# Optimization experiments

Hardware: AMD Instinct MI355X
Metric: run time of the kernel (lower is better)

The kernel has to match this reference:

```python
import jax, jax.numpy as jnp
from jax import lax
import numpy as np

B, A, D = 4, 512, 729   # batch, num_angles, detector pixels
H, W = 512, 512         # reconstruction volume


def setup_inputs() -> dict:
    key = jax.random.key(0)
    sino = jax.random.normal(key, (B, A, D), dtype=jnp.float32)
    vol_spacing = np.array([1.0, 1.0], dtype=np.float32)          # (sy, sx)
    det_spacing = np.array([1.0], dtype=np.float32)
    vol_origin = np.array([-(H - 1) / 2.0, -(W - 1) / 2.0], dtype=np.float32)
    det_origin = np.array([-(D - 1) / 2.0], dtype=np.float32)
    angles = jnp.linspace(0.0, jnp.pi, A, endpoint=False, dtype=jnp.float32)
    return {
        "input": sino,
        "volume_shape": np.array([H, W], dtype=np.int64),
        "volume_origin": jnp.asarray(vol_origin),
        "detector_origin": jnp.asarray(det_origin),
        "volume_spacing": jnpp if False else jnp.asarray(vol_spacing),
        "detector_spacing": jnp.asarray(det_spacing),
        "trajectory": angles,
    }


def _backproject(sino, vol_shape, vol_origin, det_origin, vol_spacing, det_spacing, angles):
    h, w = int(vol_shape[0]), int(vol_shape[1])
    d = sino.shape[-1]
    ys = vol_origin[0] + jnp.arange(h, dtype=sino.dtype) * vol_spacing[0]  # [H]
    xs = vol_origin[1] + jnp.arange(w, dtype=sino.dtype) * vol_spacing[1]  # [W]

    def step(acc, per_angle):
        theta, sino_a = per_angle                      # scalar, [B, D]
        # ray coordinate s = x*cos(theta) + y*sin(theta) for every voxel
        s = xs[None, :] * jnp.cos(theta) + ys[:, None] * jnp.sin(theta)  # [H, W]
        u = (s - det_origin[0]) / det_spacing[0]       # continuous detector index
        u0 = jnp.floor(u)
        frac = u - u0
        i0 = u0.astype(jnp.int32)
        i1 = i0 + 1
        valid0 = (i0 >= 0) & (i0 < d)
        valid1 = (i1 >= 0) & (i1 < d)
        i0c = jnp.clip(i0, 0, d - 1)
        i1c = jnp.clip(i1, 0, d - 1)
        v0 = sino_a[:, i0c]                            # [B, H, W] gather
        v1 = sino_a[:, i1c]                            # [B, H, W] gather
        contrib = (jnp.where(valid0, (1.0 - frac) * v0, 0.0)
                   + jnp.where(valid1, frac * v1, 0.0))
        return acc + contrib, None

    acc0 = jnp.zeros((sino.shape[0], h, w), dtype=sino.dtype)
    out, _ = lax.scan(step, acc0, (angles, jnp.swapaxes(sino, 0, 1)))
    return out


def reference(input, volume_shape, volume_origin, detector_origin,
              volume_spacing, detector_spacing, trajectory):
    return _backproject(input, volume_shape, volume_origin, detector_origin,
                        volume_spacing, detector_spacing, trajectory)
```

## Files before the change

kernel.cpp:

```cpp
#include <hip/hip_runtime.h>

#define BB 4
#define AA 512
#define ZS 4
#define AH (AA / ZS)
#define DD 729
#define HH 512
#define WW 512
#define CH 8
#define WIN 32

typedef float f4v __attribute__((ext_vector_type(4)));

__device__ inline void gload_lds(const float* g, float* l) {
    __builtin_amdgcn_global_load_lds(
        (const __attribute__((address_space(1))) unsigned int*)g,
        (__attribute__((address_space(3))) unsigned int*)l, 4, 0, 0);
}

__global__ __launch_bounds__(128, 8) void bp_kernel(
    const float* __restrict__ sino,
    const float* __restrict__ vol_origin,
    const float* __restrict__ det_origin,
    const float* __restrict__ vol_spacing,
    const float* __restrict__ det_spacing,
    const float* __restrict__ angles,
    float* __restrict__ out)
{
    __shared__ f4v   s_csk[AH];
    __shared__ int   s_s0[AH];
    __shared__ float s_win[2][CH * WIN * BB];

    const int tid  = threadIdx.y * 16 + threadIdx.x;
    const int lane = tid & 63;
    const int wv   = tid >> 6;

    const float inv_ds = 1.0f / det_spacing[0];
    const int abase = blockIdx.z * AH;

    const int x0 = blockIdx.x * 16;
    const int y0 = blockIdx.y * 16;
    const float vsx = vol_spacing[1], vsy = vol_spacing[0];
    const float off = -det_origin[0] * inv_ds;
    const float xc = vol_origin[1] + ((float)x0 + 7.5f) * vsx;
    const float yc = vol_origin[0] + ((float)y0 + 7.5f) * vsy;

    for (int a = tid; a < AH; a += 128) {
        float th = angles[abase + a];
        float c = cosf(th) * inv_ds;
        float s = sinf(th) * inv_ds;
        float uc = fmaf(xc, c, fmaf(yc, s, off));
        int s0 = min(max((int)uc - (WIN / 2), 0), DD - WIN);
        f4v k;
        k.x = c; k.y = s; k.z = off - (float)s0; k.w = 8.0f * vsy * s;
        s_csk[a] = k;
        s_s0[a]  = s0;
    }
    __syncthreads();

    const int ix  = x0 + threadIdx.x;
    const int iyA = y0 + threadIdx.y;
    const float xw = vol_origin[1] + (float)ix * vsx;
    const float yw = vol_origin[0] + (float)iyA * vsy;

    const int sidx = wv * 64 + lane;
    const long sgoff = (long)(lane & 3) * (AA * DD) + (sidx >> 2);

    f4v accA = {0.f, 0.f, 0.f, 0.f};
    f4v accB = {0.f, 0.f, 0.f, 0.f};

    #define STAGE(A0, P)                                                   \
        do {                                                               \
            _Pragma("unroll")                                              \
            for (int i = 0; i < CH; ++i) {                                 \
                const int  s0  = s_s0[(A0) + i];                           \
                const long row = (long)(abase + (A0) + i) * DD + s0;       \
                gload_lds(sino + row + sgoff,                              \
                          &s_win[P][i * (WIN * BB) + wv * 64]);            \
            }                                                              \
        } while (0)

    int p = 0;
    STAGE(0, 0);
    for (int a0 = 0; a0 < AH; a0 += CH) {
        __syncthreads();
        if (a0 + CH < AH) STAGE(a0 + CH, p ^ 1);
        #pragma unroll
        for (int j = 0; j < CH; ++j) {
            const f4v  k  = s_csk[a0 + j];
            const float u0 = fmaf(xw, k.x, fmaf(yw, k.y, k.z));
            const float u1 = u0 + k.w;
            {
                const int   li = (int)u0;
                const float fr = __builtin_amdgcn_fractf(u0);
                const float om = 1.0f - fr;
                const f4v* w = (const f4v*)&s_win[p][(j * WIN + li) * BB];
                const f4v P = w[0], Q = w[1];
                const f4v fr4 = {fr, fr, fr, fr};
                const f4v om4 = {om, om, om, om};
                accA = accA + fr4 * Q + om4 * P;
            }
            {
                const int   li = (int)u1;
                const float fr = __builtin_amdgcn_fractf(u1);
                const float om = 1.0f - fr;
                const f4v* w = (const f4v*)&s_win[p][(j * WIN + li) * BB];
                const f4v P = w[0], Q = w[1];
                const f4v fr4 = {fr, fr, fr, fr};
                const f4v om4 = {om, om, om, om};
                accB = accB + fr4 * Q + om4 * P;
            }
        }
        p ^= 1;
    }
    #undef STAGE

    const size_t HW = (size_t)HH * WW;
    const size_t oA = (size_t)iyA * WW + ix;
    const size_t oB = oA + (size_t)8 * WW;
    unsafeAtomicAdd(&out[oA],          accA.x);
    unsafeAtomicAdd(&out[oA + HW],     accA.y);
    unsafeAtomicAdd(&out[oA + 2 * HW], accA.z);
    unsafeAtomicAdd(&out[oA + 3 * HW], accA.w);
    unsafeAtomicAdd(&out[oB],          accB.x);
    unsafeAtomicAdd(&out[oB + HW],     accB.y);
    unsafeAtomicAdd(&out[oB + 2 * HW], accB.z);
    unsafeAtomicAdd(&out[oB + 3 * HW], accB.w);
}

extern "C" void kernel_launch(void* const* d_in, const int* in_sizes, int n_in,
                              void* d_out, int out_size, void* d_ws, size_t ws_size,
                              hipStream_t stream) {
    const float* sino        = (const float*)d_in[0];
    const float* vol_origin  = (const float*)d_in[2];
    const float* det_origin  = (const float*)d_in[3];
    const float* vol_spacing = (const float*)d_in[4];
    const float* det_spacing = (const float*)d_in[5];
    const float* angles      = (const float*)d_in[6];
    float* out = (float*)d_out;

    hipMemsetAsync(d_out, 0, (size_t)out_size * sizeof(float), stream);

    dim3 block(16, 8, 1);
    dim3 grid(WW / 16, HH / 16, ZS);
    bp_kernel<<<grid, block, 0, stream>>>(sino, vol_origin, det_origin,
                                          vol_spacing, det_spacing, angles, out);
}
```

Measured before the change: 136.2 us.

## Use single-wave blocks with waitcnt-based pipelining and four rows per thread

Shrinks each block to one 64-lane wavefront, so the staged LDS loads can be synchronised with s_waitcnt on the vector-memory counter alone, with no block barriers. Each thread now accumulates four output rows spaced four apart instead of two. The angle split doubles to 8 z-slices and the chunk size falls to 4 angles. The aim is to remove barrier stalls and raise per-thread reuse, at the cost of twice as many output atomics and relying on wave-level ordering for LDS visibility.

```diff
diff --git a/kernel.cpp b/kernel.cpp
--- a/kernel.cpp
+++ b/kernel.cpp
@@ -2,12 +2,13 @@
 
 #define BB 4
 #define AA 512
-#define ZS 4
+#define ZS 8
 #define AH (AA / ZS)
 #define DD 729
 #define HH 512
 #define WW 512
-#define CH 8
+#define CH 4
+#define NC (AH / CH)
 #define WIN 32
 
 typedef float f4v __attribute__((ext_vector_type(4)));
@@ -18,7 +19,10 @@
         (__attribute__((address_space(3))) unsigned int*)l, 4, 0, 0);
 }
 
-__global__ __launch_bounds__(128, 8) void bp_kernel(
+#define WAIT_VM8 0x0F78
+#define WAIT_VM0 0x0F70
+
+__global__ __launch_bounds__(64, 8) void bp_kernel(
     const float* __restrict__ sino,
     const float* __restrict__ vol_origin,
     const float* __restrict__ det_origin,
@@ -31,9 +35,7 @@
     __shared__ int   s_s0[AH];
     __shared__ float s_win[2][CH * WIN * BB];
 
-    const int tid  = threadIdx.y * 16 + threadIdx.x;
-    const int lane = tid & 63;
-    const int wv   = tid >> 6;
+    const int lane = threadIdx.y * 16 + threadIdx.x;
 
     const float inv_ds = 1.0f / det_spacing[0];
     const int abase = blockIdx.z * AH;
@@ -45,87 +47,96 @@
     const float xc = vol_origin[1] + ((float)x0 + 7.5f) * vsx;
     const float yc = vol_origin[0] + ((float)y0 + 7.5f) * vsy;
 
-    for (int a = tid; a < AH; a += 128) {
+    {
+        const int a = lane;
         float th = angles[abase + a];
         float c = cosf(th) * inv_ds;
         float s = sinf(th) * inv_ds;
         float uc = fmaf(xc, c, fmaf(yc, s, off));
         int s0 = min(max((int)uc - (WIN / 2), 0), DD - WIN);
         f4v k;
-        k.x = c; k.y = s; k.z = off - (float)s0; k.w = 8.0f * vsy * s;
+        k.x = c; k.y = s; k.z = off - (float)s0; k.w = 4.0f * vsy * s;
         s_csk[a] = k;
         s_s0[a]  = s0;
     }
-    __syncthreads();
+    __builtin_amdgcn_s_waitcnt(0xC070);
 
     const int ix  = x0 + threadIdx.x;
-    const int iyA = y0 + threadIdx.y;
+    const int iy0 = y0 + threadIdx.y;
     const float xw = vol_origin[1] + (float)ix * vsx;
-    const float yw = vol_origin[0] + (float)iyA * vsy;
+    const float yw = vol_origin[0] + (float)iy0 * vsy;
 
-    const int sidx = wv * 64 + lane;
-    const long sgoff = (long)(lane & 3) * (AA * DD) + (sidx >> 2);
+    const long sg0 = (long)(lane & 3) * (AA * DD) + (lane >> 2);
 
-    f4v accA = {0.f, 0.f, 0.f, 0.f};
-    f4v accB = {0.f, 0.f, 0.f, 0.f};
+    f4v acc0 = {0.f, 0.f, 0.f, 0.f};
+    f4v acc1 = {0.f, 0.f, 0.f, 0.f};
+    f4v acc2 = {0.f, 0.f, 0.f, 0.f};
+    f4v acc3 = {0.f, 0.f, 0.f, 0.f};
 
-    #define STAGE(A0, P)                                                   \
+    #define STAGE(C, P)                                                    \
         do {                                                               \
             _Pragma("unroll")                                              \
             for (int i = 0; i < CH; ++i) {                                 \
-                const int  s0  = s_s0[(A0) + i];                           \
-                const long row = (long)(abase + (A0) + i) * DD + s0;       \
-                gload_lds(sino + row + sgoff,                              \
-                          &s_win[P][i * (WIN * BB) + wv * 64]);            \
+                const int  aa  = (C) * CH + i;                             \
+                const long row = (long)(abase + aa) * DD + s_s0[aa];       \
+                float* dst = &s_win[P][i * (WIN * BB)];                    \
+                gload_lds(sino + row + sg0, dst);                          \
+                gload_lds(sino + row + sg0 + 16, dst + 64);                \
             }                                                              \
+        } while (0)
+
+    #define LERP(U, ACC)                                                   \
+        do {                                                               \
+            const int   li = (int)(U);                                     \
+            const float fr = __builtin_amdgcn_fractf(U);                   \
+            const float om = 1.0f - fr;                                    \
+            const f4v* w = (const f4v*)&s_win[p][(j * WIN + li) * BB];     \
+            const f4v P = w[0], Q = w[1];                                  \
+            const f4v fr4 = {fr, fr, fr, fr};                              \
+            const f4v om4 = {om, om, om, om};                              \
+            ACC = ACC + fr4 * Q + om4 * P;                                 \
         } while (0)
 
     int p = 0;
     STAGE(0, 0);
-    for (int a0 = 0; a0 < AH; a0 += CH) {
-        __syncthreads();
-        if (a0 + CH < AH) STAGE(a0 + CH, p ^ 1);
+    for (int c = 0; c < NC; ++c) {
+        if (c + 1 < NC) {
+            STAGE(c + 1, p ^ 1);
+            __builtin_amdgcn_s_waitcnt(WAIT_VM8);
+        } else {
+            __builtin_amdgcn_s_waitcnt(WAIT_VM0);
+        }
         #pragma unroll
         for (int j = 0; j < CH; ++j) {
-            const f4v  k  = s_csk[a0 + j];
+            const f4v  k  = s_csk[c * CH + j];
             const float u0 = fmaf(xw, k.x, fmaf(yw, k.y, k.z));
             const float u1 = u0 + k.w;
-            {
-                const int   li = (int)u0;
-                const float fr = __builtin_amdgcn_fractf(u0);
-                const float om = 1.0f - fr;
-                const f4v* w = (const f4v*)&s_win[p][(j * WIN + li) * BB];
-                const f4v P = w[0], Q = w[1];
-                const f4v fr4 = {fr, fr, fr, fr};
-                const f4v om4 = {om, om, om, om};
-                accA = accA + fr4 * Q + om4 * P;
-            }
-            {
-                const int   li = (int)u1;
-                const float fr = __builtin_amdgcn_fractf(u1);
-                const float om = 1.0f - fr;
-                const f4v* w = (const f4v*)&s_win[p][(j * WIN + li) * BB];
-                const f4v P = w[0], Q = w[1];
-                const f4v fr4 = {fr, fr, fr, fr};
-                const f4v om4 = {om, om, om, om};
-                accB = accB + fr4 * Q + om4 * P;
-            }
+            const float u2 = u1 + k.w;
+            const float u3 = u2 + k.w;
+            LERP(u0, acc0);
+            LERP(u1, acc1);
+            LERP(u2, acc2);
+            LERP(u3, acc3);
         }
         p ^= 1;
     }
     #undef STAGE
+    #undef LERP
 
     const size_t HW = (size_t)HH * WW;
-    const size_t oA = (size_t)iyA * WW + ix;
-    const size_t oB = oA + (size_t)8 * WW;
-    unsafeAtomicAdd(&out[oA],          accA.x);
-    unsafeAtomicAdd(&out[oA + HW],     accA.y);
-    unsafeAtomicAdd(&out[oA + 2 * HW], accA.z);
-    unsafeAtomicAdd(&out[oA + 3 * HW], accA.w);
-    unsafeAtomicAdd(&out[oB],          accB.x);
-    unsafeAtomicAdd(&out[oB + HW],     accB.y);
-    unsafeAtomicAdd(&out[oB + 2 * HW], accB.z);
-    unsafeAtomicAdd(&out[oB + 3 * HW], accB.w);
+    #define OUT4(ACC, ROWOFF)                                              \
+        do {                                                               \
+            const size_t o = (size_t)(iy0 + (ROWOFF)) * WW + ix;           \
+            unsafeAtomicAdd(&out[o],          (ACC).x);                    \
+            unsafeAtomicAdd(&out[o + HW],     (ACC).y);                    \
+            unsafeAtomicAdd(&out[o + 2 * HW], (ACC).z);                    \
+            unsafeAtomicAdd(&out[o + 3 * HW], (ACC).w);                    \
+        } while (0)
+    OUT4(acc0, 0);
+    OUT4(acc1, 4);
+    OUT4(acc2, 8);
+    OUT4(acc3, 12);
+    #undef OUT4
 }
 
 extern "C" void kernel_launch(void* const* d_in, const int* in_sizes, int n_in,
@@ -141,7 +152,7 @@
 
     hipMemsetAsync(d_out, 0, (size_t)out_size * sizeof(float), stream);
 
-    dim3 block(16, 8, 1);
+    dim3 block(16, 4, 1);
     dim3 grid(WW / 16, HH / 16, ZS);
     bp_kernel<<<grid, block, 0, stream>>>(sino, vol_origin, det_origin,
                                           vol_spacing, det_spacing, angles, out);
```

Result: slower. 139.7 us (+2.5%).
